# Kernel optimization log

Measured on AMD Instinct MI355X. Metric: run time of the kernel, lower is better.

## Reference

```python
import jax, jax.numpy as jnp
import numpy as np


def setup_inputs() -> dict:
    key = jax.random.key(0)
    ks = jax.random.split(key, 6)
    B, S, DK = 4, 2048, 1024
    scale = 1.0 / np.sqrt(DK)  # keep weight magnitudes sane like torch init
    return {
        "q": jax.random.normal(ks[0], (B, S, DK), jnp.float32),
        "k": jax.random.normal(ks[1], (B, S, DK), jnp.float32),
        "v": jax.random.normal(ks[2], (B, S, DK), jnp.float32),
        "wq": jax.random.normal(ks[3], (DK, DK), jnp.float32) * scale,
        "wk": jax.random.normal(ks[4], (DK, DK), jnp.float32) * scale,
        "wv": jax.random.normal(ks[5], (DK, DK), jnp.float32) * scale,
    }


def reference(q, k, v, wq, wk, wv):
    dk = q.shape[-1]
    # nn.Linear: y = x @ W^T  (weights stored [out, in])
    qp = jnp.einsum("bsd,ed->bse", q, wq)
    kp = jnp.einsum("bsd,ed->bse", k, wk)
    vp = jnp.einsum("bsd,ed->bse", v, wv)
    norm = 1.0 / jnp.sqrt(jnp.asarray(dk, qp.dtype))
    s = jnp.einsum("bqd,bkd->bqk", qp, kp) * norm  # [B, S, S]
    # module computes exp(s)/sum(exp(s)) manually; mathematically softmax
    e = jnp.exp(s)
    attention = e / jnp.sum(e, axis=-1, keepdims=True)
    # dropout is identity in eval mode (deterministic reference)
    return jnp.einsum("bqk,bkd->bqd", attention, vp)
```

## Files before the change

### kernel.cpp

```cpp
#include <hip/hip_runtime.h>

typedef _Float16 f16;
typedef _Float16 f16x4 __attribute__((ext_vector_type(4)));
typedef _Float16 f16x8 __attribute__((ext_vector_type(8)));
typedef float    fx4   __attribute__((ext_vector_type(4)));

#define MODE_PROJ   0
#define MODE_SCORES 1
#define MODE_PV     2

constexpr int Bsz = 4;
constexpr int S   = 2048;
constexpr int DK  = 1024;
constexpr int BM = 128, BN = 128, BK = 64;
constexpr long SD   = (long)S * DK;
constexpr long SS   = (long)S * S;
constexpr long BIGN = (long)Bsz * S * DK;

__device__ __forceinline__ void glds16(const f16* g, f16* l) {
    __builtin_amdgcn_global_load_lds(
        (const __attribute__((address_space(1))) void*)g,
        (__attribute__((address_space(3))) void*)l, 16, 0, 0);
}

__global__ __launch_bounds__(256)
void convert_kernel(const float* q, const float* k, const float* v,
                    const float* wq, const float* wk, const float* wv)
{
    int bx = blockIdx.x;
    const float* src;
    int blk;
    if (bx < 12288) {
        int t = bx >> 12; blk = bx & 4095;
        src = (t == 0) ? q : (t == 1) ? k : v;
    } else {
        int u = bx - 12288;
        int t = u >> 9; blk = u & 511;
        src = (t == 0) ? wq : (t == 1) ? wk : wv;
    }
    size_t off = (size_t)blk * 2048 + (size_t)threadIdx.x * 8;
    float4 f0 = *(const float4*)(src + off);
    float4 f1 = *(const float4*)(src + off + 4);
    __syncthreads();
    f16x8 h = {(f16)f0.x, (f16)f0.y, (f16)f0.z, (f16)f0.w,
               (f16)f1.x, (f16)f1.y, (f16)f1.z, (f16)f1.w};
    *(f16x8*)((char*)src + (size_t)blk * 8192 + (size_t)threadIdx.x * 16) = h;
}

__device__ __forceinline__ size_t pp(int r, int c) {
    return ((size_t)(r >> 1) << 12) + ((r & 1) << 10) + c;
}

template<int MODE>
__global__ __launch_bounds__(256, 4)
void gemm_kernel(const f16* A0, const f16* A1, const f16* A2,
                 const f16* B0, const f16* B1, const f16* B2,
                 void* O0, void* O1, float* rowsum,
                 int lda, int ldb, int K, int ldo)
{
    __shared__ f16 lA[BM * BK];
    __shared__ f16 lB[BN * BK];

    const int tid = threadIdx.x;
    const int id  = blockIdx.x;
    const int z   = blockIdx.y;
    int row0, col0;
    if constexpr (MODE == MODE_PROJ) { row0 = (id & 63) * BM; col0 = (id >> 6) * BN; }
    else                             { row0 = (id & 15) * BM; col0 = (id >> 4) * BN; }

    const int lane = tid & 63;
    const int quad = lane >> 4;
    const int cn   = lane & 15;
    const int w    = tid >> 6;
    const int wm   = w >> 1;
    const int wn   = w & 1;

    const f16 *Ap, *Bp;
    if constexpr (MODE == MODE_PROJ) {
        Ap = (z == 0) ? A0 : (z == 1) ? A1 : A2;
        Bp = (z == 0) ? B0 : (z == 1) ? B1 : B2;
    } else if constexpr (MODE == MODE_SCORES) {
        Ap = A0 + (long)z * SD;  Bp = B0 + (long)z * SD;
        rowsum += (long)z * S;
    } else {
        Ap = A0 + (long)z * SS;  Bp = B0 + (long)z * SD;
        rowsum += (long)z * S;
    }

    fx4 acc[4][4];
    #pragma unroll
    for (int mt = 0; mt < 4; ++mt)
        #pragma unroll
        for (int nt = 0; nt < 4; ++nt)
            acc[mt][nt] = (fx4){0.f, 0.f, 0.f, 0.f};

    const int lr8 = lane >> 3;
    const int swc = (lane & 7) ^ lr8;
    const int lcS = swc << 3;

    for (int k0 = 0; k0 < K; k0 += BK) {
        __syncthreads();
        #pragma unroll
        for (int i = 0; i < 4; ++i) {
            int rb = w * 32 + i * 8;
            if constexpr (MODE == MODE_PROJ) {
                glds16(Ap + pp(row0 + rb + lr8, k0 + lcS), &lA[rb * BK]);
                glds16(Bp + pp(col0 + rb + lr8, k0 + lcS), &lB[rb * BK]);
            } else {
                glds16(Ap + (size_t)(row0 + rb + lr8) * lda + k0 + lcS, &lA[rb * BK]);
                glds16(Bp + (size_t)(col0 + rb + lr8) * ldb + k0 + lcS, &lB[rb * BK]);
            }
        }
        __syncthreads();

        #pragma unroll
        for (int kh = 0; kh < 2; ++kh) {
            f16x8 af[4], bf[4];
            #pragma unroll
            for (int mt = 0; mt < 4; ++mt) {
                int r = wm * 64 + mt * 16 + cn;
                int ch = ((kh << 2) | quad) ^ (r & 7);
                af[mt] = *(const f16x8*)&lA[r * BK + ch * 8];
            }
            #pragma unroll
            for (int nt = 0; nt < 4; ++nt) {
                int r = wn * 64 + nt * 16 + cn;
                int ch = ((kh << 2) | quad) ^ (r & 7);
                bf[nt] = *(const f16x8*)&lB[r * BK + ch * 8];
            }
            #pragma unroll
            for (int mt = 0; mt < 4; ++mt)
                #pragma unroll
                for (int nt = 0; nt < 4; ++nt)
                    acc[mt][nt] = __builtin_amdgcn_mfma_f32_16x16x32_f16(
                        af[mt], bf[nt], acc[mt][nt], 0, 0, 0);
        }
    }

    if constexpr (MODE == MODE_PROJ) {
        if (z < 2) {
            f16* O = (f16*)O0 + (long)z * BIGN;
            #pragma unroll
            for (int mt = 0; mt < 4; ++mt) {
                int r0 = row0 + wm * 64 + mt * 16 + quad * 4;
                #pragma unroll
                for (int nt = 0; nt < 4; ++nt) {
                    int c = col0 + wn * 64 + nt * 16 + cn;
                    #pragma unroll
                    for (int reg = 0; reg < 4; ++reg)
                        O[(size_t)(r0 + reg) * DK + c] = (f16)acc[mt][nt][reg];
                }
            }
        } else {
            #pragma unroll
            for (int mt = 0; mt < 4; ++mt) {
                int r0 = row0 + wm * 64 + mt * 16 + quad * 4;
                int b  = r0 >> 11;
                int s  = r0 & 2047;
                f16* O = (f16*)O1 + (long)b * SD;
                #pragma unroll
                for (int nt = 0; nt < 4; ++nt) {
                    int c = col0 + wn * 64 + nt * 16 + cn;
                    f16x4 h = {(f16)acc[mt][nt][0], (f16)acc[mt][nt][1],
                               (f16)acc[mt][nt][2], (f16)acc[mt][nt][3]};
                    *(f16x4*)&O[(size_t)c * S + s] = h;
                }
            }
        }
    } else if constexpr (MODE == MODE_SCORES) {
        f16* O = (f16*)O0 + (long)z * SS;
        const float sl2e = 0.03125f * 1.44269504f;
        float rs[4][4];
        #pragma unroll
        for (int mt = 0; mt < 4; ++mt)
            #pragma unroll
            for (int reg = 0; reg < 4; ++reg) rs[mt][reg] = 0.f;
        #pragma unroll
        for (int mt = 0; mt < 4; ++mt) {
            int r0 = row0 + wm * 64 + mt * 16 + quad * 4;
            #pragma unroll
            for (int nt = 0; nt < 4; ++nt) {
                int c = col0 + wn * 64 + nt * 16 + cn;
                #pragma unroll
                for (int reg = 0; reg < 4; ++reg) {
                    float vv = exp2f(acc[mt][nt][reg] * sl2e);
                    rs[mt][reg] += vv;
                    O[(size_t)(r0 + reg) * ldo + c] = (f16)vv;
                }
            }
        }
        #pragma unroll
        for (int mt = 0; mt < 4; ++mt) {
            int r0 = row0 + wm * 64 + mt * 16 + quad * 4;
            #pragma unroll
            for (int reg = 0; reg < 4; ++reg) {
                float vv = rs[mt][reg];
                vv += __shfl_xor(vv, 1);
                vv += __shfl_xor(vv, 2);
                vv += __shfl_xor(vv, 4);
                vv += __shfl_xor(vv, 8);
                if (cn == 0) atomicAdd(&rowsum[r0 + reg], vv);
            }
        }
    } else {
        float* O = (float*)O0 + (long)z * SD;
        #pragma unroll
        for (int mt = 0; mt < 4; ++mt) {
            int r0 = row0 + wm * 64 + mt * 16 + quad * 4;
            fx4 rsv = *(const fx4*)&rowsum[r0];
            fx4 inv = {1.f / rsv[0], 1.f / rsv[1], 1.f / rsv[2], 1.f / rsv[3]};
            #pragma unroll
            for (int nt = 0; nt < 4; ++nt) {
                int c = col0 + wn * 64 + nt * 16 + cn;
                #pragma unroll
                for (int reg = 0; reg < 4; ++reg)
                    O[(size_t)(r0 + reg) * ldo + c] = acc[mt][nt][reg] * inv[reg];
            }
        }
    }
}

extern "C" void kernel_launch(void* const* d_in, const int* in_sizes, int n_in,
                              void* d_out, int out_size, void* d_ws, size_t ws_size,
                              hipStream_t stream) {
    const float* q  = (const float*)d_in[0];
    const float* k  = (const float*)d_in[1];
    const float* v  = (const float*)d_in[2];
    const float* wq = (const float*)d_in[3];
    const float* wk = (const float*)d_in[4];
    const float* wv = (const float*)d_in[5];
    float* out = (float*)d_out;

    char* ws = (char*)d_ws;
    f16*   qp     = (f16*)(ws);
    f16*   kp     = (f16*)(ws + ((size_t)16 << 20));
    f16*   vpT    = (f16*)(ws + ((size_t)32 << 20));
    f16*   E      = (f16*)(ws + ((size_t)48 << 20));
    float* rowsum = (float*)(ws + ((size_t)80 << 20));

    hipMemsetAsync(rowsum, 0, (size_t)Bsz * S * sizeof(float), stream);

    convert_kernel<<<13824, 256, 0, stream>>>(q, k, v, wq, wk, wv);

    const f16* qh  = (const f16*)q;
    const f16* kh  = (const f16*)k;
    const f16* vh  = (const f16*)v;
    const f16* wqh = (const f16*)wq;
    const f16* wkh = (const f16*)wk;
    const f16* wvh = (const f16*)wv;

    dim3 blk(256);
    gemm_kernel<MODE_PROJ><<<dim3(512, 3), blk, 0, stream>>>(
        qh, kh, vh, wqh, wkh, wvh, qp, vpT, nullptr, DK, DK, DK, DK);
    gemm_kernel<MODE_SCORES><<<dim3(256, 4), blk, 0, stream>>>(
        qp, nullptr, nullptr, kp, nullptr, nullptr, E, nullptr, rowsum,
        DK, DK, DK, S);
    gemm_kernel<MODE_PV><<<dim3(128, 4), blk, 0, stream>>>(
        E, nullptr, nullptr, vpT, nullptr, nullptr, out, nullptr, rowsum,
        S, S, S, DK);
}
```

Baseline: 298.8 us.

## Fuse fp32-to-fp16 conversion of q/k/v into projection GEMM A-tile loads

Stops converting the q, k and v activations into fp16 in place with a separate pass. The projection GEMM now reads fp32 activations directly, converts them in registers and writes swizzled fp16 into LDS. Only the weights are pre-converted into workspace, and the rowsum memset is folded into that same small kernel. This removes a full read/write pass over the activations and one launch. In exchange, the projection GEMM loses its async global-to-LDS path for A, doubles A's global bytes per tile, and its occupancy hint drops from 4 to 3 blocks.

```diff
diff --git a/kernel.cpp b/kernel.cpp
--- a/kernel.cpp
+++ b/kernel.cpp
@@ -24,37 +24,34 @@
 }
 
 __global__ __launch_bounds__(256)
-void convert_kernel(const float* q, const float* k, const float* v,
-                    const float* wq, const float* wk, const float* wv)
+void wconvert_kernel(const float* wq, const float* wk, const float* wv,
+                     f16* wqh, f16* wkh, f16* wvh, float* rowsum)
 {
     int bx = blockIdx.x;
-    const float* src;
-    int blk;
-    if (bx < 12288) {
-        int t = bx >> 12; blk = bx & 4095;
-        src = (t == 0) ? q : (t == 1) ? k : v;
+    if (bx < 1536) {
+        int t = bx >> 9, blk = bx & 511;
+        const float* src = (t == 0) ? wq : (t == 1) ? wk : wv;
+        f16*         dst = (t == 0) ? wqh : (t == 1) ? wkh : wvh;
+        size_t off = (size_t)blk * 2048 + (size_t)threadIdx.x * 8;
+        float4 f0 = *(const float4*)(src + off);
+        float4 f1 = *(const float4*)(src + off + 4);
+        f16x8 h = {(f16)f0.x, (f16)f0.y, (f16)f0.z, (f16)f0.w,
+                   (f16)f1.x, (f16)f1.y, (f16)f1.z, (f16)f1.w};
+        *(f16x8*)(dst + off) = h;
     } else {
-        int u = bx - 12288;
-        int t = u >> 9; blk = u & 511;
-        src = (t == 0) ? wq : (t == 1) ? wk : wv;
-    }
-    size_t off = (size_t)blk * 2048 + (size_t)threadIdx.x * 8;
-    float4 f0 = *(const float4*)(src + off);
-    float4 f1 = *(const float4*)(src + off + 4);
-    __syncthreads();
-    f16x8 h = {(f16)f0.x, (f16)f0.y, (f16)f0.z, (f16)f0.w,
-               (f16)f1.x, (f16)f1.y, (f16)f1.z, (f16)f1.w};
-    *(f16x8*)((char*)src + (size_t)blk * 8192 + (size_t)threadIdx.x * 16) = h;
-}
-
-__device__ __forceinline__ size_t pp(int r, int c) {
-    return ((size_t)(r >> 1) << 12) + ((r & 1) << 10) + c;
+        int blk = bx - 1536;
+        size_t off = (size_t)blk * 2048 + (size_t)threadIdx.x * 8;
+        fx4 z4 = {0.f, 0.f, 0.f, 0.f};
+        *(fx4*)(rowsum + off)     = z4;
+        *(fx4*)(rowsum + off + 4) = z4;
+    }
 }
 
 template<int MODE>
-__global__ __launch_bounds__(256, 4)
-void gemm_kernel(const f16* A0, const f16* A1, const f16* A2,
+__global__ __launch_bounds__(256, 3)
+void gemm_kernel(const float* Fq, const float* Fk, const float* Fv,
                  const f16* B0, const f16* B1, const f16* B2,
+                 const f16* A0,
                  void* O0, void* O1, float* rowsum,
                  int lda, int ldb, int K, int ldo)
 {
@@ -75,10 +72,11 @@
     const int wm   = w >> 1;
     const int wn   = w & 1;
 
-    const f16 *Ap, *Bp;
+    const float* Afp = nullptr;
+    const f16 *Ap = nullptr, *Bp;
     if constexpr (MODE == MODE_PROJ) {
-        Ap = (z == 0) ? A0 : (z == 1) ? A1 : A2;
-        Bp = (z == 0) ? B0 : (z == 1) ? B1 : B2;
+        Afp = (z == 0) ? Fq : (z == 1) ? Fk : Fv;
+        Bp  = (z == 0) ? B0 : (z == 1) ? B1 : B2;
     } else if constexpr (MODE == MODE_SCORES) {
         Ap = A0 + (long)z * SD;  Bp = B0 + (long)z * SD;
         rowsum += (long)z * S;
@@ -95,18 +93,32 @@
             acc[mt][nt] = (fx4){0.f, 0.f, 0.f, 0.f};
 
     const int lr8 = lane >> 3;
-    const int swc = (lane & 7) ^ lr8;
-    const int lcS = swc << 3;
+    const int lcS = ((lane & 7) ^ lr8) << 3;
 
     for (int k0 = 0; k0 < K; k0 += BK) {
         __syncthreads();
-        #pragma unroll
-        for (int i = 0; i < 4; ++i) {
-            int rb = w * 32 + i * 8;
-            if constexpr (MODE == MODE_PROJ) {
-                glds16(Ap + pp(row0 + rb + lr8, k0 + lcS), &lA[rb * BK]);
-                glds16(Bp + pp(col0 + rb + lr8, k0 + lcS), &lB[rb * BK]);
-            } else {
+        if constexpr (MODE == MODE_PROJ) {
+            #pragma unroll
+            for (int i = 0; i < 4; ++i) {
+                int rb = w * 32 + i * 8;
+                glds16(Bp + (size_t)(col0 + rb + lr8) * ldb + k0 + lcS, &lB[rb * BK]);
+            }
+            #pragma unroll
+            for (int i = 0; i < 4; ++i) {
+                int idx = tid + i * 256;
+                int r   = idx >> 3;
+                int ch  = idx & 7;
+                const float* src = Afp + (size_t)(row0 + r) * lda + k0 + ch * 8;
+                float4 a0 = *(const float4*)src;
+                float4 a1 = *(const float4*)(src + 4);
+                f16x8 h = {(f16)a0.x, (f16)a0.y, (f16)a0.z, (f16)a0.w,
+                           (f16)a1.x, (f16)a1.y, (f16)a1.z, (f16)a1.w};
+                *(f16x8*)&lA[r * BK + ((ch ^ (r & 7)) << 3)] = h;
+            }
+        } else {
+            #pragma unroll
+            for (int i = 0; i < 4; ++i) {
+                int rb = w * 32 + i * 8;
                 glds16(Ap + (size_t)(row0 + rb + lr8) * lda + k0 + lcS, &lA[rb * BK]);
                 glds16(Bp + (size_t)(col0 + rb + lr8) * ldb + k0 + lcS, &lB[rb * BK]);
             }
@@ -237,25 +249,19 @@
     f16*   vpT    = (f16*)(ws + ((size_t)32 << 20));
     f16*   E      = (f16*)(ws + ((size_t)48 << 20));
     float* rowsum = (float*)(ws + ((size_t)80 << 20));
-
-    hipMemsetAsync(rowsum, 0, (size_t)Bsz * S * sizeof(float), stream);
-
-    convert_kernel<<<13824, 256, 0, stream>>>(q, k, v, wq, wk, wv);
-
-    const f16* qh  = (const f16*)q;
-    const f16* kh  = (const f16*)k;
-    const f16* vh  = (const f16*)v;
-    const f16* wqh = (const f16*)wq;
-    const f16* wkh = (const f16*)wk;
-    const f16* wvh = (const f16*)wv;
+    f16*   wqh    = (f16*)(ws + ((size_t)81 << 20));
+    f16*   wkh    = (f16*)(ws + ((size_t)83 << 20));
+    f16*   wvh    = (f16*)(ws + ((size_t)85 << 20));
+
+    wconvert_kernel<<<1540, 256, 0, stream>>>(wq, wk, wv, wqh, wkh, wvh, rowsum);
 
     dim3 blk(256);
     gemm_kernel<MODE_PROJ><<<dim3(512, 3), blk, 0, stream>>>(
-        qh, kh, vh, wqh, wkh, wvh, qp, vpT, nullptr, DK, DK, DK, DK);
+        q, k, v, wqh, wkh, wvh, nullptr, qp, vpT, nullptr, DK, DK, DK, DK);
     gemm_kernel<MODE_SCORES><<<dim3(256, 4), blk, 0, stream>>>(
-        qp, nullptr, nullptr, kp, nullptr, nullptr, E, nullptr, rowsum,
+        nullptr, nullptr, nullptr, kp, nullptr, nullptr, qp, E, nullptr, rowsum,
         DK, DK, DK, S);
     gemm_kernel<MODE_PV><<<dim3(128, 4), blk, 0, stream>>>(
-        E, nullptr, nullptr, vpT, nullptr, nullptr, out, nullptr, rowsum,
+        nullptr, nullptr, nullptr, vpT, nullptr, nullptr, E, out, nullptr, rowsum,
         S, S, S, DK);
 }
```

Result: slower. 314.8 us (+5.3%).
